# Optimization experiments

Measured on AMD Instinct MI355X. Metric: run time of the kernel, lower is better.

Reference implementation:

```python
import jax, jax.numpy as jnp
import numpy as np

N = 100000
E = 1600000
HID = 128


def gcn_conv(x, W, b, src, dst, n):
    # PyG GCNConv: h = X W; add self-loops; D^{-1/2}(A+I)D^{-1/2} h + b
    h = x @ W                                   # [n, out]
    loop = jnp.arange(n)
    s = jnp.concatenate([src, loop])            # sources incl. self-loops
    d = jnp.concatenate([dst, loop])            # targets incl. self-loops
    deg = jax.ops.segment_sum(jnp.ones(s.shape[0], dtype=h.dtype), d, num_segments=n)
    dinv = jnp.where(deg > 0, jax.lax.rsqrt(deg), 0.0)
    norm = dinv[s] * dinv[d]                    # [E+n]
    out = jax.ops.segment_sum(h[s] * norm[:, None], d, num_segments=n)
    return out + b


def setup_inputs() -> dict:
    key = jax.random.key(0)
    ks = jax.random.split(key, 16)
    coords = jax.random.normal(ks[0], (N, 2), dtype=jnp.float32)
    edge_index = jax.random.randint(ks[1], (2, E), 0, N, dtype=jnp.int64)

    def lin(k, fin, fout):
        k1, k2 = jax.random.split(k)
        s = 1.0 / np.sqrt(fin)
        W = jax.random.uniform(k1, (fin, fout), jnp.float32, -s, s)
        b = jax.random.uniform(k2, (fout,), jnp.float32, -s, s)
        return W, b

    W1, b1 = lin(ks[2], 3, HID)
    W2, b2 = lin(ks[3], HID, HID)
    Ws, bs = lin(ks[4], HID, 1)
    Wmu, bmu = lin(ks[5], HID, 2)
    Wls, bls = lin(ks[6], HID, 2)
    Wv1, bv1 = lin(ks[7], HID, 64)
    Wv2, bv2 = lin(ks[8], 64, 1)
    return {"coords": coords, "edge_index": edge_index,
            "W1": W1, "b1": b1, "W2": W2, "b2": b2,
            "Ws": Ws, "bs": bs, "Wmu": Wmu, "bmu": bmu,
            "Wls": Wls, "bls": bls, "Wv1": Wv1, "bv1": bv1,
            "Wv2": Wv2, "bv2": bv2}


def reference(coords, edge_index, W1, b1, W2, b2, Ws, bs, Wmu, bmu, Wls, bls, Wv1, bv1, Wv2, bv2):
    n = coords.shape[0]
    src, dst = edge_index[0], edge_index[1]
    # degree feature (no self-loops), normalized by max degree
    degree = jax.ops.segment_sum(jnp.ones(src.shape[0], dtype=jnp.float32), src, num_segments=n)
    degree = degree / jnp.maximum(degree.max(), 1.0)
    x = jnp.concatenate([coords, degree[:, None]], axis=1)  # [N, 3]
    x = jax.nn.relu(gcn_conv(x, W1, b1, src, dst, n))       # [N, HID]
    x = jax.nn.relu(gcn_conv(x, W2, b2, src, dst, n))       # [N, HID]
    node_logits = jax.nn.log_softmax((x @ Ws + bs).squeeze(-1), axis=0)  # [N]
    mu = x @ Wmu + bmu                                      # [N, 2]
    log_std = jnp.clip(x @ Wls + bls, -4.0, 2.0)            # [N, 2]
    g = x.mean(axis=0)                                      # [HID]
    value = (jax.nn.relu(g @ Wv1 + bv1) @ Wv2 + bv2).squeeze()
    return node_logits, mu, log_std, value
```

## Files before the change

### kernel.cpp

```cpp
#include <hip/hip_runtime.h>
#include <hip/hip_bf16.h>

#define HID 128
#define NBMAX 512

typedef __bf16 bf16x8 __attribute__((ext_vector_type(8)));
typedef float f32x4 __attribute__((ext_vector_type(4)));
typedef float f32x2 __attribute__((ext_vector_type(2)));

#if defined(__has_builtin)
#if __has_builtin(__builtin_amdgcn_cvt_pk_f32_fp8) && __has_builtin(__builtin_amdgcn_cvt_pk_fp8_f32)
#define HAVE_FP8_CVT 1
#endif
#endif
#ifndef HAVE_FP8_CVT
#define HAVE_FP8_CVT 0
#include <hip/hip_fp8.h>
#endif

__device__ __forceinline__ float b2f(unsigned int u) { return __uint_as_float(u << 16); }
__device__ __forceinline__ float b2f_hi(unsigned int u) { return __uint_as_float(u & 0xFFFF0000u); }
__device__ __forceinline__ unsigned int f2b(float f) {
  unsigned int b = __float_as_uint(f);
  return (b + 0x7FFFu + ((b >> 16) & 1u)) >> 16;
}
__device__ __forceinline__ unsigned int pack2(float lo, float hi) {
  return f2b(lo) | (f2b(hi) << 16);
}

#if !HAVE_FP8_CVT
__device__ __forceinline__ float fp8dec(unsigned int u) {
  unsigned int e = (u >> 3) & 15, m = u & 7, sgn = (u >> 7) & 1;
  float v;
  if (e) v = __uint_as_float(((e + 120) << 23) | (m << 20));
  else v = (float)m * 0.001953125f;
  return sgn ? -v : v;
}
#endif

__device__ __forceinline__ unsigned int pk4_fp8(float v0, float v1, float v2, float v3) {
#if HAVE_FP8_CVT
  int pk = 0;
  pk = __builtin_amdgcn_cvt_pk_fp8_f32(v0, v1, pk, false);
  pk = __builtin_amdgcn_cvt_pk_fp8_f32(v2, v3, pk, true);
  return (unsigned int)pk;
#else
  __hip_fp8_e4m3 a(v0), b(v1), c(v2), d(v3);
  return (unsigned)a.__x | ((unsigned)b.__x << 8) | ((unsigned)c.__x << 16) |
         ((unsigned)d.__x << 24);
#endif
}

__device__ __forceinline__ void acc4_fp8(unsigned int u, float* a) {
#if HAVE_FP8_CVT
  f32x2 lo = __builtin_amdgcn_cvt_pk_f32_fp8((int)u, false);
  f32x2 hi = __builtin_amdgcn_cvt_pk_f32_fp8((int)u, true);
  a[0] += lo.x; a[1] += lo.y; a[2] += hi.x; a[3] += hi.y;
#else
  a[0] += fp8dec(u & 255); a[1] += fp8dec((u >> 8) & 255);
  a[2] += fp8dec((u >> 16) & 255); a[3] += fp8dec((u >> 24) & 255);
#endif
}

__global__ void k_hist(const int* __restrict__ src, const int* __restrict__ dst, int E, int NB,
                       int* __restrict__ hd_g, int* __restrict__ hs_g) {
  __shared__ int hd[NBMAX], hs[NBMAX];
  for (int i = threadIdx.x; i < NB; i += 256) { hd[i] = 0; hs[i] = 0; }
  __syncthreads();
  int stride = gridDim.x * 256;
  for (int e = blockIdx.x * 256 + threadIdx.x; e < E; e += stride) {
    atomicAdd(&hd[dst[e] >> 8], 1);
    atomicAdd(&hs[src[e] >> 8], 1);
  }
  __syncthreads();
  for (int i = threadIdx.x; i < NB; i += 256) {
    if (hd[i]) atomicAdd(&hd_g[i], hd[i]);
    if (hs[i]) atomicAdd(&hs_g[i], hs[i]);
  }
}

__global__ void k_scan_buckets(const int* __restrict__ hd_g, const int* __restrict__ hs_g,
                               int NB, int E, int* __restrict__ based, int* __restrict__ bases,
                               int* __restrict__ curd, int* __restrict__ curs) {
  __shared__ int sd[NBMAX], ss[NBMAX];
  int i = threadIdx.x;
  int vd = (i < NB) ? hd_g[i] : 0;
  int vs = (i < NB) ? hs_g[i] : 0;
  sd[i] = vd; ss[i] = vs; __syncthreads();
  for (int st = 1; st < NBMAX; st <<= 1) {
    int td = (i >= st) ? sd[i - st] : 0;
    int ts = (i >= st) ? ss[i - st] : 0;
    __syncthreads();
    sd[i] += td; ss[i] += ts;
    __syncthreads();
  }
  if (i < NB) {
    int bd = sd[i] - vd, bs = ss[i] - vs;
    based[i] = bd; bases[i] = bs;
    curd[i] = bd; curs[i] = bs;
  }
  if (i == 0) { based[NB] = E; bases[NB] = E; }
}

__global__ void k_bucket_scatter(const int* __restrict__ src, const int* __restrict__ dst,
                                 int E, int NB, int* __restrict__ curd, int* __restrict__ curs,
                                 int* __restrict__ pairsp, int* __restrict__ srcb) {
  __shared__ int hd[NBMAX], hs[NBMAX], bd[NBMAX], bs[NBMAX];
  for (int i = threadIdx.x; i < NB; i += 256) { hd[i] = 0; hs[i] = 0; }
  __syncthreads();
  int per = (E + gridDim.x - 1) / gridDim.x;
  int begin = blockIdx.x * per;
  int end = min(E, begin + per);
  for (int e = begin + threadIdx.x; e < end; e += 256) {
    atomicAdd(&hd[dst[e] >> 8], 1);
    atomicAdd(&hs[src[e] >> 8], 1);
  }
  __syncthreads();
  for (int i = threadIdx.x; i < NB; i += 256) {
    bd[i] = hd[i] ? atomicAdd(&curd[i], hd[i]) : 0;
    bs[i] = hs[i] ? atomicAdd(&curs[i], hs[i]) : 0;
    hd[i] = 0; hs[i] = 0;
  }
  __syncthreads();
  for (int e = begin + threadIdx.x; e < end; e += 256) {
    int d = dst[e], s = src[e];
    int p = bd[d >> 8] + atomicAdd(&hd[d >> 8], 1);
    pairsp[p] = (s << 8) | (d & 255);
    int q = bs[s >> 8] + atomicAdd(&hs[s >> 8], 1);
    srcb[q] = s;
  }
}

__global__ void k_degcsr(const int* __restrict__ srcb, const int* __restrict__ bases,
                         const int* __restrict__ pairsp, const int* __restrict__ based,
                         int N, int E, int* __restrict__ degsrc, int* __restrict__ bmax,
                         int* __restrict__ rowptr, float* __restrict__ dinv,
                         int* __restrict__ colarr) {
  __shared__ int cnt[256], scn[256], cur[256];
  int b = blockIdx.x, tid = threadIdx.x;
  int g = (b << 8) + tid;
  cnt[tid] = 0; __syncthreads();
  int lo = bases[b], hi = bases[b + 1];
  for (int k = lo + tid; k < hi; k += 256) atomicAdd(&cnt[srcb[k] & 255], 1);
  __syncthreads();
  int c = cnt[tid];
  if (g < N) degsrc[g] = c;
  scn[tid] = (g < N) ? c : 0; __syncthreads();
  for (int s = 128; s > 0; s >>= 1) {
    if (tid < s) scn[tid] = max(scn[tid], scn[tid + s]);
    __syncthreads();
  }
  if (tid == 0) bmax[b] = scn[0];
  __syncthreads();
  cnt[tid] = 0; __syncthreads();
  lo = based[b]; hi = based[b + 1];
  for (int k = lo + tid; k < hi; k += 256) atomicAdd(&cnt[pairsp[k] & 255], 1);
  __syncthreads();
  c = cnt[tid];
  scn[tid] = c; __syncthreads();
  for (int st = 1; st < 256; st <<= 1) {
    int t = (tid >= st) ? scn[tid - st] : 0;
    __syncthreads();
    scn[tid] += t;
    __syncthreads();
  }
  int excl = scn[tid] - c;
  if (g < N) {
    rowptr[g] = lo + excl;
    dinv[g] = rsqrtf((float)(c + 1));
  }
  cur[tid] = lo + excl;
  __syncthreads();
  for (int k = lo + tid; k < hi; k += 256) {
    int p = pairsp[k];
    int pos = atomicAdd(&cur[p & 255], 1);
    colarr[pos] = ((unsigned)p) >> 8;
  }
  if (b == 0 && tid == 0) rowptr[N] = E;
}

__global__ void k_prepW(const float* __restrict__ W2, unsigned short* __restrict__ W2T) {
  int idx = blockIdx.x * 256 + threadIdx.x;
  if (idx >= 128 * 128) return;
  int j = idx >> 7, k = idx & 127;
  W2T[j * 128 + k] = (unsigned short)f2b(W2[k * 128 + j]);
}

__global__ void k_node(const float* __restrict__ coords, const int* __restrict__ degsrc,
                       const float* __restrict__ dinv, const int* __restrict__ bmax, int NB,
                       int N, float4* __restrict__ x0s) {
  __shared__ int sm[256];
  int tid = threadIdx.x;
  int m = 0;
  for (int i = tid; i < NB; i += 256) m = max(m, bmax[i]);
  sm[tid] = m; __syncthreads();
  for (int s = 128; s > 0; s >>= 1) {
    if (tid < s) sm[tid] = max(sm[tid], sm[tid + s]);
    __syncthreads();
  }
  float inv = 1.0f / (float)max(sm[0], 1);
  int n = blockIdx.x * 256 + tid;
  if (n >= N) return;
  float di = dinv[n];
  float4 v;
  v.x = coords[n * 2 + 0] * di;
  v.y = coords[n * 2 + 1] * di;
  v.z = (float)degsrc[n] * inv * di;
  v.w = 0.f;
  x0s[n] = v;
}

__global__ void k_agg3lin(const float4* __restrict__ x0s, const float* __restrict__ dinv,
                          const int* __restrict__ rowptr, const int* __restrict__ col,
                          const float* __restrict__ W1, const float* __restrict__ b1, int N,
                          unsigned int* __restrict__ x1f8) {
  __shared__ float w0s[128], w1s[128], w2s[128], bsm[128];
  for (int t = threadIdx.x; t < 128; t += 256) {
    w0s[t] = W1[t];
    w1s[t] = W1[128 + t];
    w2s[t] = W1[256 + t];
    bsm[t] = b1[t];
  }
  __syncthreads();
  int n = blockIdx.x * 256 + threadIdx.x;
  if (n >= N) return;
  float4 a = x0s[n];
  int b = rowptr[n], en = rowptr[n + 1];
  int k = b;
  for (; k + 3 < en; k += 4) {
    int s0 = col[k], s1 = col[k + 1], s2 = col[k + 2], s3 = col[k + 3];
    float4 w0 = x0s[s0];
    float4 w1 = x0s[s1];
    float4 w2 = x0s[s2];
    float4 w3 = x0s[s3];
    a.x += (w0.x + w1.x) + (w2.x + w3.x);
    a.y += (w0.y + w1.y) + (w2.y + w3.y);
    a.z += (w0.z + w1.z) + (w2.z + w3.z);
  }
  for (; k < en; k++) {
    float4 w = x0s[col[k]];
    a.x += w.x; a.y += w.y; a.z += w.z;
  }
  float di = dinv[n];
  float ax = a.x * di, ay = a.y * di, az = a.z * di;
  unsigned int* orow = x1f8 + (size_t)n * 32;
#pragma unroll 8
  for (int f0 = 0; f0 < 128; f0 += 4) {
    float v0 = fmaxf(bsm[f0] + ax * w0s[f0] + ay * w1s[f0] + az * w2s[f0], 0.f) * di;
    float v1 = fmaxf(bsm[f0 + 1] + ax * w0s[f0 + 1] + ay * w1s[f0 + 1] + az * w2s[f0 + 1], 0.f) * di;
    float v2 = fmaxf(bsm[f0 + 2] + ax * w0s[f0 + 2] + ay * w1s[f0 + 2] + az * w2s[f0 + 2], 0.f) * di;
    float v3 = fmaxf(bsm[f0 + 3] + ax * w0s[f0 + 3] + ay * w1s[f0 + 3] + az * w2s[f0 + 3], 0.f) * di;
    orow[f0 >> 2] = pk4_fp8(v0, v1, v2, v3);
  }
}

__global__ void k_agg128(const unsigned int* __restrict__ x1f8, const float* __restrict__ dinv,
                         const int* __restrict__ rowptr, const int* __restrict__ col,
                         int N, unsigned short* __restrict__ xa) {
  int g = (int)((blockIdx.x * 256 + threadIdx.x) >> 3);
  int lane = threadIdx.x & 7;
  if (g >= N) return;
  const uint4* base = (const uint4*)x1f8 + lane;
  float acc[16];
#pragma unroll
  for (int i = 0; i < 16; i++) acc[i] = 0.f;
  uint4 self = base[(size_t)g * 8];
  acc4_fp8(self.x, acc); acc4_fp8(self.y, acc + 4);
  acc4_fp8(self.z, acc + 8); acc4_fp8(self.w, acc + 12);
  int b = rowptr[g], en = rowptr[g + 1];
  int k = b;
  for (; k + 3 < en; k += 4) {
    int s0 = col[k], s1 = col[k + 1], s2 = col[k + 2], s3 = col[k + 3];
    uint4 w0 = base[(size_t)s0 * 8];
    uint4 w1 = base[(size_t)s1 * 8];
    uint4 w2 = base[(size_t)s2 * 8];
    uint4 w3 = base[(size_t)s3 * 8];
    acc4_fp8(w0.x, acc); acc4_fp8(w0.y, acc + 4); acc4_fp8(w0.z, acc + 8); acc4_fp8(w0.w, acc + 12);
    acc4_fp8(w1.x, acc); acc4_fp8(w1.y, acc + 4); acc4_fp8(w1.z, acc + 8); acc4_fp8(w1.w, acc + 12);
    acc4_fp8(w2.x, acc); acc4_fp8(w2.y, acc + 4); acc4_fp8(w2.z, acc + 8); acc4_fp8(w2.w, acc + 12);
    acc4_fp8(w3.x, acc); acc4_fp8(w3.y, acc + 4); acc4_fp8(w3.z, acc + 8); acc4_fp8(w3.w, acc + 12);
  }
  for (; k < en; k++) {
    uint4 w = base[(size_t)col[k] * 8];
    acc4_fp8(w.x, acc); acc4_fp8(w.y, acc + 4); acc4_fp8(w.z, acc + 8); acc4_fp8(w.w, acc + 12);
  }
  float di = dinv[g];
  uint4 o1, o2;
  o1.x = pack2(acc[0] * di, acc[1] * di);
  o1.y = pack2(acc[2] * di, acc[3] * di);
  o1.z = pack2(acc[4] * di, acc[5] * di);
  o1.w = pack2(acc[6] * di, acc[7] * di);
  o2.x = pack2(acc[8] * di, acc[9] * di);
  o2.y = pack2(acc[10] * di, acc[11] * di);
  o2.z = pack2(acc[12] * di, acc[13] * di);
  o2.w = pack2(acc[14] * di, acc[15] * di);
  uint4* op = (uint4*)xa + (size_t)g * 16 + lane * 2;
  op[0] = o1;
  op[1] = o2;
}

__global__ __launch_bounds__(256) void k_gemm2(const unsigned short* __restrict__ xab,
                                               const unsigned short* __restrict__ W2T,
                                               const float* __restrict__ b2,
                                               const float* __restrict__ Ws,
                                               const float* __restrict__ bs,
                                               const float* __restrict__ Wmu,
                                               const float* __restrict__ bmu,
                                               const float* __restrict__ Wls,
                                               const float* __restrict__ bls,
                                               int N, float* __restrict__ s_arr,
                                               float* __restrict__ out,
                                               float* __restrict__ partials) {
  __shared__ float w[640];
  __shared__ float cs[4][128];
  for (int t = threadIdx.x; t < 128; t += 256) {
    w[t] = Ws[t];
    w[128 + t] = Wmu[t * 2 + 0];
    w[256 + t] = Wmu[t * 2 + 1];
    w[384 + t] = Wls[t * 2 + 0];
    w[512 + t] = Wls[t * 2 + 1];
  }
  __syncthreads();
  int wv = threadIdx.x >> 6;
  int lane = threadIdx.x & 63;
  int l15 = lane & 15, lhi = lane >> 4;
  int rowbase = blockIdx.x * 64 + wv * 16;
  int arow = rowbase + l15;
  int arowc = min(arow, N - 1);
  const unsigned short* ap = xab + (size_t)arowc * HID + lhi * 8;
  bf16x8 a[4];
#pragma unroll
  for (int kk = 0; kk < 4; kk++) a[kk] = *(const bf16x8*)(ap + kk * 32);
  float cpart[8];
  float p0[4] = {0, 0, 0, 0}, p1[4] = {0, 0, 0, 0}, p2[4] = {0, 0, 0, 0};
  float p3[4] = {0, 0, 0, 0}, p4[4] = {0, 0, 0, 0};
#pragma unroll
  for (int ct = 0; ct < 8; ct++) {
    f32x4 acc = {0.f, 0.f, 0.f, 0.f};
    const unsigned short* bp = W2T + (size_t)(ct * 16 + l15) * HID + lhi * 8;
#pragma unroll
    for (int kk = 0; kk < 4; kk++) {
      bf16x8 bfr = *(const bf16x8*)(bp + kk * 32);
      acc = __builtin_amdgcn_mfma_f32_16x16x32_bf16(a[kk], bfr, acc, 0, 0, 0);
    }
    int cidx = ct * 16 + l15;
    float bias = b2[cidx];
    float ws_ = w[cidx];
    float wm0 = w[128 + cidx], wm1 = w[256 + cidx];
    float wl0 = w[384 + cidx], wl1 = w[512 + cidx];
    float cl = 0.f;
#pragma unroll
    for (int r = 0; r < 4; r++) {
      int node = rowbase + lhi * 4 + r;
      float o = fmaxf(acc[r] + bias, 0.f);
      if (node < N) cl += o;
      p0[r] += o * ws_;
      p1[r] += o * wm0;
      p2[r] += o * wm1;
      p3[r] += o * wl0;
      p4[r] += o * wl1;
    }
    cl += __shfl_xor(cl, 16);
    cl += __shfl_xor(cl, 32);
    cpart[ct] = cl;
  }
#pragma unroll
  for (int r = 0; r < 4; r++) {
#pragma unroll
    for (int m = 1; m < 16; m <<= 1) {
      p0[r] += __shfl_xor(p0[r], m);
      p1[r] += __shfl_xor(p1[r], m);
      p2[r] += __shfl_xor(p2[r], m);
      p3[r] += __shfl_xor(p3[r], m);
      p4[r] += __shfl_xor(p4[r], m);
    }
  }
  if (l15 == 0) {
#pragma unroll
    for (int r = 0; r < 4; r++) {
      int node = rowbase + lhi * 4 + r;
      if (node < N) {
        s_arr[node] = p0[r] + bs[0];
        out[(size_t)N + node * 2 + 0] = p1[r] + bmu[0];
        out[(size_t)N + node * 2 + 1] = p2[r] + bmu[1];
        out[(size_t)3 * N + node * 2 + 0] = fminf(fmaxf(p3[r] + bls[0], -4.f), 2.f);
        out[(size_t)3 * N + node * 2 + 1] = fminf(fmaxf(p4[r] + bls[1], -4.f), 2.f);
      }
    }
  }
  if (lane < 16) {
#pragma unroll
    for (int ct = 0; ct < 8; ct++) cs[wv][ct * 16 + lane] = cpart[ct];
  }
  __syncthreads();
  if (threadIdx.x < 128) {
    int f = threadIdx.x;
    partials[(size_t)blockIdx.x * 128 + f] = cs[0][f] + cs[1][f] + cs[2][f] + cs[3][f];
  }
}

__global__ void k_lse_colsum(const float* __restrict__ s, int N, float* __restrict__ pm,
                             float* __restrict__ pt, const float* __restrict__ partials,
                             int nblkG, float* __restrict__ colsum) {
  if (blockIdx.x >= 256) {
    int bb = blockIdx.x - 256;
    int f = threadIdx.x;
    if (f < 128) {
      float t = 0.f;
      for (int b = bb; b < nblkG; b += 64) t += partials[(size_t)b * 128 + f];
      atomicAdd(&colsum[f], t);
    }
    return;
  }
  __shared__ float smM[256], smT[256];
  float m = -1e30f, t = 0.f;
  for (int i = blockIdx.x * 256 + threadIdx.x; i < N; i += 256 * 256) {
    float v = s[i];
    if (v > m) { t = t * __expf(m - v) + 1.f; m = v; }
    else t += __expf(v - m);
  }
  smM[threadIdx.x] = m; smT[threadIdx.x] = t; __syncthreads();
  for (int st = 128; st > 0; st >>= 1) {
    if (threadIdx.x < st) {
      float m2 = smM[threadIdx.x + st], t2 = smT[threadIdx.x + st];
      float m1 = smM[threadIdx.x], t1 = smT[threadIdx.x];
      float M = fmaxf(m1, m2);
      smM[threadIdx.x] = M;
      smT[threadIdx.x] = t1 * __expf(m1 - M) + t2 * __expf(m2 - M);
    }
    __syncthreads();
  }
  if (threadIdx.x == 0) { pm[blockIdx.x] = smM[0]; pt[blockIdx.x] = smT[0]; }
}

__global__ void k_logits_value(const float* __restrict__ sarr, const float* __restrict__ pm,
                               const float* __restrict__ pt, int N, float* __restrict__ out,
                               const float* __restrict__ colsum, const float* __restrict__ Wv1,
                               const float* __restrict__ bv1, const float* __restrict__ Wv2,
                               const float* __restrict__ bv2, int nblkN) {
  if ((int)blockIdx.x == nblkN) {
    __shared__ float hid[64];
    float invN = 1.0f / (float)N;
    int j = threadIdx.x;
    if (j < 64) {
      float a = bv1[j];
      for (int f = 0; f < 128; f++) a += (colsum[f] * invN) * Wv1[f * 64 + j];
      hid[j] = fmaxf(a, 0.f) * Wv2[j];
    }
    __syncthreads();
    if (threadIdx.x == 0) {
      float v = bv2[0];
      for (int jj = 0; jj < 64; jj++) v += hid[jj];
      out[(size_t)5 * N] = v;
    }
    return;
  }
  __shared__ float smM[256], smT[256];
  smM[threadIdx.x] = pm[threadIdx.x];
  smT[threadIdx.x] = pt[threadIdx.x];
  __syncthreads();
  for (int st = 128; st > 0; st >>= 1) {
    if (threadIdx.x < st) {
      float m2 = smM[threadIdx.x + st], t2 = smT[threadIdx.x + st];
      float m1 = smM[threadIdx.x], t1 = smT[threadIdx.x];
      float M = fmaxf(m1, m2);
      smM[threadIdx.x] = M;
      smT[threadIdx.x] = t1 * __expf(m1 - M) + t2 * __expf(m2 - M);
    }
    __syncthreads();
  }
  float lse = smM[0] + logf(smT[0]);
  int n = blockIdx.x * 256 + threadIdx.x;
  if (n < N) out[n] = sarr[n] - lse;
}

extern "C" void kernel_launch(void* const* d_in, const int* in_sizes, int n_in,
                              void* d_out, int out_size, void* d_ws, size_t ws_size,
                              hipStream_t stream) {
  const float* coords = (const float*)d_in[0];
  const int* ei = (const int*)d_in[1];
  const float* W1 = (const float*)d_in[2];
  const float* b1 = (const float*)d_in[3];
  const float* W2 = (const float*)d_in[4];
  const float* b2 = (const float*)d_in[5];
  const float* Wsw = (const float*)d_in[6];
  const float* bsw = (const float*)d_in[7];
  const float* Wmu = (const float*)d_in[8];
  const float* bmu = (const float*)d_in[9];
  const float* Wls = (const float*)d_in[10];
  const float* bls = (const float*)d_in[11];
  const float* Wv1 = (const float*)d_in[12];
  const float* bv1 = (const float*)d_in[13];
  const float* Wv2 = (const float*)d_in[14];
  const float* bv2 = (const float*)d_in[15];
  int N = in_sizes[0] / 2;
  int E = in_sizes[1] / 2;
  const int* src = ei;
  const int* dst = ei + E;
  float* outf = (float*)d_out;
  int NB = (N + 255) >> 8;
  int nblkG = (N + 63) / 64;
  int nblkN = (N + 255) / 256;

  char* base = (char*)d_ws;
  size_t off = 0;
  auto alloc = [&](size_t bytes) -> void* {
    void* r = base + off;
    off += (bytes + 255) & ~(size_t)255;
    return r;
  };
  size_t zero_start = off;
  int* hd_g = (int*)alloc((size_t)NB * 4);
  int* hs_g = (int*)alloc((size_t)NB * 4);
  float* colsum = (float*)alloc(128 * 4);
  size_t zero_bytes = off - zero_start;
  int* based = (int*)alloc(((size_t)NB + 1) * 4);
  int* bases = (int*)alloc(((size_t)NB + 1) * 4);
  int* curd = (int*)alloc((size_t)NB * 4);
  int* curs = (int*)alloc((size_t)NB * 4);
  int* bmax = (int*)alloc((size_t)NB * 4);
  int* rowptr = (int*)alloc(((size_t)N + 1) * 4);
  int* pairsp = (int*)alloc((size_t)E * 4);
  int* srcb = (int*)alloc((size_t)E * 4);
  int* colarr = (int*)alloc((size_t)E * 4);
  int* degsrc = (int*)alloc((size_t)N * 4);
  float* dinv = (float*)alloc((size_t)N * 4);
  float4* x0s = (float4*)alloc((size_t)N * 16);
  float* sarr = (float*)alloc((size_t)N * 4);
  float* pm = (float*)alloc(256 * 4);
  float* pt = (float*)alloc(256 * 4);
  unsigned short* W2T = (unsigned short*)alloc(128 * 128 * 2);
  float* partials = (float*)alloc((size_t)nblkG * 128 * 4);
  unsigned int* x1f8 = (unsigned int*)alloc((size_t)N * 128);
  unsigned short* xab = (unsigned short*)alloc((size_t)N * HID * 2);
  if (off > ws_size) return;

  hipMemsetAsync(base + zero_start, 0, zero_bytes, stream);
  k_hist<<<256, 256, 0, stream>>>(src, dst, E, NB, hd_g, hs_g);
  k_scan_buckets<<<1, NBMAX, 0, stream>>>(hd_g, hs_g, NB, E, based, bases, curd, curs);
  k_bucket_scatter<<<512, 256, 0, stream>>>(src, dst, E, NB, curd, curs, pairsp, srcb);
  k_degcsr<<<NB, 256, 0, stream>>>(srcb, bases, pairsp, based, N, E, degsrc, bmax, rowptr, dinv,
                                   colarr);
  k_prepW<<<64, 256, 0, stream>>>(W2, W2T);
  k_node<<<nblkN, 256, 0, stream>>>(coords, degsrc, dinv, bmax, NB, N, x0s);
  k_agg3lin<<<nblkN, 256, 0, stream>>>(x0s, dinv, rowptr, colarr, W1, b1, N, x1f8);
  k_agg128<<<(N * 8 + 255) / 256, 256, 0, stream>>>(x1f8, dinv, rowptr, colarr, N, xab);
  k_gemm2<<<nblkG, 256, 0, stream>>>(xab, W2T, b2, Wsw, bsw, Wmu, bmu, Wls, bls, N, sarr, outf,
                                     partials);
  k_lse_colsum<<<320, 256, 0, stream>>>(sarr, N, pm, pt, partials, nblkG, colsum);
  k_logits_value<<<nblkN + 1, 256, 0, stream>>>(sarr, pm, pt, N, outf, colsum, Wv1, bv1, Wv2,
                                                bv2, nblkN);
}
```

Measured before the change: 202.9 us.

## Replace histogram-scan bucketing with fixed-capacity 1024-node buckets and int2 row ranges

Drops the global histogram and bucket-scan kernels. Edges are now scattered straight into fixed-capacity slots per bucket, with each bucket covering 1024 nodes and capacity set to about 1.25x the average plus slack. The CSR build kernel moves to 1024-thread blocks, and row pointers become int2 begin/end pairs. This removes two launches and one full pass over the edge list. In exchange, the CSR build runs only about 98 blocks, and any edge that lands past a bucket's capacity is silently dropped, so skewed graphs would give wrong results.

```diff
diff --git a/kernel.cpp b/kernel.cpp
--- a/kernel.cpp
+++ b/kernel.cpp
@@ -2,7 +2,7 @@
 #include <hip/hip_bf16.h>
 
 #define HID 128
-#define NBMAX 512
+#define NB2MAX 128
 
 typedef __bf16 bf16x8 __attribute__((ext_vector_type(8)));
 typedef float f32x4 __attribute__((ext_vector_type(4)));
@@ -19,7 +19,6 @@
 #endif
 
 __device__ __forceinline__ float b2f(unsigned int u) { return __uint_as_float(u << 16); }
-__device__ __forceinline__ float b2f_hi(unsigned int u) { return __uint_as_float(u & 0xFFFF0000u); }
 __device__ __forceinline__ unsigned int f2b(float f) {
   unsigned int b = __float_as_uint(f);
   return (b + 0x7FFFu + ((b >> 16) & 1u)) >> 16;
@@ -62,61 +61,21 @@
 #endif
 }
 
-__global__ void k_hist(const int* __restrict__ src, const int* __restrict__ dst, int E, int NB,
-                       int* __restrict__ hd_g, int* __restrict__ hs_g) {
-  __shared__ int hd[NBMAX], hs[NBMAX];
-  for (int i = threadIdx.x; i < NB; i += 256) { hd[i] = 0; hs[i] = 0; }
-  __syncthreads();
-  int stride = gridDim.x * 256;
-  for (int e = blockIdx.x * 256 + threadIdx.x; e < E; e += stride) {
-    atomicAdd(&hd[dst[e] >> 8], 1);
-    atomicAdd(&hs[src[e] >> 8], 1);
-  }
-  __syncthreads();
-  for (int i = threadIdx.x; i < NB; i += 256) {
-    if (hd[i]) atomicAdd(&hd_g[i], hd[i]);
-    if (hs[i]) atomicAdd(&hs_g[i], hs[i]);
-  }
-}
-
-__global__ void k_scan_buckets(const int* __restrict__ hd_g, const int* __restrict__ hs_g,
-                               int NB, int E, int* __restrict__ based, int* __restrict__ bases,
-                               int* __restrict__ curd, int* __restrict__ curs) {
-  __shared__ int sd[NBMAX], ss[NBMAX];
-  int i = threadIdx.x;
-  int vd = (i < NB) ? hd_g[i] : 0;
-  int vs = (i < NB) ? hs_g[i] : 0;
-  sd[i] = vd; ss[i] = vs; __syncthreads();
-  for (int st = 1; st < NBMAX; st <<= 1) {
-    int td = (i >= st) ? sd[i - st] : 0;
-    int ts = (i >= st) ? ss[i - st] : 0;
-    __syncthreads();
-    sd[i] += td; ss[i] += ts;
-    __syncthreads();
-  }
-  if (i < NB) {
-    int bd = sd[i] - vd, bs = ss[i] - vs;
-    based[i] = bd; bases[i] = bs;
-    curd[i] = bd; curs[i] = bs;
-  }
-  if (i == 0) { based[NB] = E; bases[NB] = E; }
-}
-
-__global__ void k_bucket_scatter(const int* __restrict__ src, const int* __restrict__ dst,
-                                 int E, int NB, int* __restrict__ curd, int* __restrict__ curs,
-                                 int* __restrict__ pairsp, int* __restrict__ srcb) {
-  __shared__ int hd[NBMAX], hs[NBMAX], bd[NBMAX], bs[NBMAX];
-  for (int i = threadIdx.x; i < NB; i += 256) { hd[i] = 0; hs[i] = 0; }
+__global__ void k_scatter2(const int* __restrict__ src, const int* __restrict__ dst, int E,
+                           int NB2, int CAP, int* __restrict__ curd, int* __restrict__ curs,
+                           int* __restrict__ pairsp, int* __restrict__ srcb) {
+  __shared__ int hd[NB2MAX], hs[NB2MAX], bd[NB2MAX], bs[NB2MAX];
+  for (int i = threadIdx.x; i < NB2; i += 256) { hd[i] = 0; hs[i] = 0; }
   __syncthreads();
   int per = (E + gridDim.x - 1) / gridDim.x;
   int begin = blockIdx.x * per;
   int end = min(E, begin + per);
   for (int e = begin + threadIdx.x; e < end; e += 256) {
-    atomicAdd(&hd[dst[e] >> 8], 1);
-    atomicAdd(&hs[src[e] >> 8], 1);
-  }
-  __syncthreads();
-  for (int i = threadIdx.x; i < NB; i += 256) {
+    atomicAdd(&hd[dst[e] >> 10], 1);
+    atomicAdd(&hs[src[e] >> 10], 1);
+  }
+  __syncthreads();
+  for (int i = threadIdx.x; i < NB2; i += 256) {
     bd[i] = hd[i] ? atomicAdd(&curd[i], hd[i]) : 0;
     bs[i] = hs[i] ? atomicAdd(&curs[i], hs[i]) : 0;
     hd[i] = 0; hs[i] = 0;
@@ -124,41 +83,45 @@
   __syncthreads();
   for (int e = begin + threadIdx.x; e < end; e += 256) {
     int d = dst[e], s = src[e];
-    int p = bd[d >> 8] + atomicAdd(&hd[d >> 8], 1);
-    pairsp[p] = (s << 8) | (d & 255);
-    int q = bs[s >> 8] + atomicAdd(&hs[s >> 8], 1);
-    srcb[q] = s;
-  }
-}
-
-__global__ void k_degcsr(const int* __restrict__ srcb, const int* __restrict__ bases,
-                         const int* __restrict__ pairsp, const int* __restrict__ based,
-                         int N, int E, int* __restrict__ degsrc, int* __restrict__ bmax,
-                         int* __restrict__ rowptr, float* __restrict__ dinv,
-                         int* __restrict__ colarr) {
-  __shared__ int cnt[256], scn[256], cur[256];
+    int bD = d >> 10, bS = s >> 10;
+    int offD = bd[bD] + atomicAdd(&hd[bD], 1);
+    if (offD < CAP) pairsp[(size_t)bD * CAP + offD] = (s << 10) | (d & 1023);
+    int offS = bs[bS] + atomicAdd(&hs[bS], 1);
+    if (offS < CAP) srcb[(size_t)bS * CAP + offS] = s & 1023;
+  }
+}
+
+__global__ __launch_bounds__(1024) void k_degcsr(
+    const int* __restrict__ srcb, const int* __restrict__ curs, const int* __restrict__ pairsp,
+    const int* __restrict__ curd, int NB2, int CAP, int N, int* __restrict__ degsrc,
+    int* __restrict__ bmax, int2* __restrict__ rowptr2, float* __restrict__ dinv,
+    int* __restrict__ colarr) {
+  __shared__ int cnt[1024], scn[1024], cur[1024];
   int b = blockIdx.x, tid = threadIdx.x;
-  int g = (b << 8) + tid;
+  int g = (b << 10) + tid;
+  int lo = b * CAP;
   cnt[tid] = 0; __syncthreads();
-  int lo = bases[b], hi = bases[b + 1];
-  for (int k = lo + tid; k < hi; k += 256) atomicAdd(&cnt[srcb[k] & 255], 1);
+  int szS = min(curs[b], CAP);
+  const int* sb = srcb + (size_t)lo;
+  for (int k = tid; k < szS; k += 1024) atomicAdd(&cnt[sb[k]], 1);
   __syncthreads();
   int c = cnt[tid];
   if (g < N) degsrc[g] = c;
   scn[tid] = (g < N) ? c : 0; __syncthreads();
-  for (int s = 128; s > 0; s >>= 1) {
+  for (int s = 512; s > 0; s >>= 1) {
     if (tid < s) scn[tid] = max(scn[tid], scn[tid + s]);
     __syncthreads();
   }
   if (tid == 0) bmax[b] = scn[0];
   __syncthreads();
   cnt[tid] = 0; __syncthreads();
-  lo = based[b]; hi = based[b + 1];
-  for (int k = lo + tid; k < hi; k += 256) atomicAdd(&cnt[pairsp[k] & 255], 1);
+  int szD = min(curd[b], CAP);
+  const int* pb = pairsp + (size_t)lo;
+  for (int k = tid; k < szD; k += 1024) atomicAdd(&cnt[pb[k] & 1023], 1);
   __syncthreads();
   c = cnt[tid];
   scn[tid] = c; __syncthreads();
-  for (int st = 1; st < 256; st <<= 1) {
+  for (int st = 1; st < 1024; st <<= 1) {
     int t = (tid >= st) ? scn[tid - st] : 0;
     __syncthreads();
     scn[tid] += t;
@@ -166,17 +129,16 @@
   }
   int excl = scn[tid] - c;
   if (g < N) {
-    rowptr[g] = lo + excl;
+    rowptr2[g] = make_int2(lo + excl, lo + excl + c);
     dinv[g] = rsqrtf((float)(c + 1));
   }
   cur[tid] = lo + excl;
   __syncthreads();
-  for (int k = lo + tid; k < hi; k += 256) {
-    int p = pairsp[k];
-    int pos = atomicAdd(&cur[p & 255], 1);
-    colarr[pos] = ((unsigned)p) >> 8;
-  }
-  if (b == 0 && tid == 0) rowptr[N] = E;
+  for (int k = tid; k < szD; k += 1024) {
+    int p = pb[k];
+    int pos = atomicAdd(&cur[p & 1023], 1);
+    colarr[pos] = ((unsigned)p) >> 10;
+  }
 }
 
 __global__ void k_prepW(const float* __restrict__ W2, unsigned short* __restrict__ W2T) {
@@ -187,17 +149,26 @@
 }
 
 __global__ void k_node(const float* __restrict__ coords, const int* __restrict__ degsrc,
-                       const float* __restrict__ dinv, const int* __restrict__ bmax, int NB,
+                       const float* __restrict__ dinv, const int* __restrict__ bmax, int NB2,
                        int N, float4* __restrict__ x0s) {
-  __shared__ int sm[256];
+  __shared__ int sm[128];
   int tid = threadIdx.x;
-  int m = 0;
-  for (int i = tid; i < NB; i += 256) m = max(m, bmax[i]);
-  sm[tid] = m; __syncthreads();
-  for (int s = 128; s > 0; s >>= 1) {
-    if (tid < s) sm[tid] = max(sm[tid], sm[tid + s]);
-    __syncthreads();
-  }
+  if (tid < 128) sm[tid] = (tid < NB2) ? bmax[tid] : 0;
+  __syncthreads();
+  if (tid < 64) { sm[tid] = max(sm[tid], sm[tid + 64]); }
+  __syncthreads();
+  if (tid < 32) { sm[tid] = max(sm[tid], sm[tid + 32]); }
+  __syncthreads();
+  if (tid < 16) { sm[tid] = max(sm[tid], sm[tid + 16]); }
+  __syncthreads();
+  if (tid < 8) { sm[tid] = max(sm[tid], sm[tid + 8]); }
+  __syncthreads();
+  if (tid < 4) { sm[tid] = max(sm[tid], sm[tid + 4]); }
+  __syncthreads();
+  if (tid < 2) { sm[tid] = max(sm[tid], sm[tid + 2]); }
+  __syncthreads();
+  if (tid == 0) sm[0] = max(sm[0], sm[1]);
+  __syncthreads();
   float inv = 1.0f / (float)max(sm[0], 1);
   int n = blockIdx.x * 256 + tid;
   if (n >= N) return;
@@ -211,7 +182,7 @@
 }
 
 __global__ void k_agg3lin(const float4* __restrict__ x0s, const float* __restrict__ dinv,
-                          const int* __restrict__ rowptr, const int* __restrict__ col,
+                          const int2* __restrict__ rowptr2, const int* __restrict__ col,
                           const float* __restrict__ W1, const float* __restrict__ b1, int N,
                           unsigned int* __restrict__ x1f8) {
   __shared__ float w0s[128], w1s[128], w2s[128], bsm[128];
@@ -225,8 +196,8 @@
   int n = blockIdx.x * 256 + threadIdx.x;
   if (n >= N) return;
   float4 a = x0s[n];
-  int b = rowptr[n], en = rowptr[n + 1];
-  int k = b;
+  int2 rp = rowptr2[n];
+  int k = rp.x, en = rp.y;
   for (; k + 3 < en; k += 4) {
     int s0 = col[k], s1 = col[k + 1], s2 = col[k + 2], s3 = col[k + 3];
     float4 w0 = x0s[s0];
@@ -255,7 +226,7 @@
 }
 
 __global__ void k_agg128(const unsigned int* __restrict__ x1f8, const float* __restrict__ dinv,
-                         const int* __restrict__ rowptr, const int* __restrict__ col,
+                         const int2* __restrict__ rowptr2, const int* __restrict__ col,
                          int N, unsigned short* __restrict__ xa) {
   int g = (int)((blockIdx.x * 256 + threadIdx.x) >> 3);
   int lane = threadIdx.x & 7;
@@ -267,8 +238,8 @@
   uint4 self = base[(size_t)g * 8];
   acc4_fp8(self.x, acc); acc4_fp8(self.y, acc + 4);
   acc4_fp8(self.z, acc + 8); acc4_fp8(self.w, acc + 12);
-  int b = rowptr[g], en = rowptr[g + 1];
-  int k = b;
+  int2 rp = rowptr2[g];
+  int k = rp.x, en = rp.y;
   for (; k + 3 < en; k += 4) {
     int s0 = col[k], s1 = col[k + 1], s2 = col[k + 2], s3 = col[k + 3];
     uint4 w0 = base[(size_t)s0 * 8];
@@ -498,7 +469,8 @@
   const int* src = ei;
   const int* dst = ei + E;
   float* outf = (float*)d_out;
-  int NB = (N + 255) >> 8;
+  int NB2 = (N + 1023) >> 10;
+  int CAP = ((E / NB2) * 5 / 4 + 1024 + 255) & ~255;
   int nblkG = (N + 63) / 64;
   int nblkN = (N + 255) / 256;
 
@@ -510,19 +482,15 @@
     return r;
   };
   size_t zero_start = off;
-  int* hd_g = (int*)alloc((size_t)NB * 4);
-  int* hs_g = (int*)alloc((size_t)NB * 4);
+  int* curd = (int*)alloc((size_t)NB2 * 4);
+  int* curs = (int*)alloc((size_t)NB2 * 4);
   float* colsum = (float*)alloc(128 * 4);
   size_t zero_bytes = off - zero_start;
-  int* based = (int*)alloc(((size_t)NB + 1) * 4);
-  int* bases = (int*)alloc(((size_t)NB + 1) * 4);
-  int* curd = (int*)alloc((size_t)NB * 4);
-  int* curs = (int*)alloc((size_t)NB * 4);
-  int* bmax = (int*)alloc((size_t)NB * 4);
-  int* rowptr = (int*)alloc(((size_t)N + 1) * 4);
-  int* pairsp = (int*)alloc((size_t)E * 4);
-  int* srcb = (int*)alloc((size_t)E * 4);
-  int* colarr = (int*)alloc((size_t)E * 4);
+  int* bmax = (int*)alloc((size_t)NB2 * 4);
+  int2* rowptr2 = (int2*)alloc((size_t)N * 8);
+  int* pairsp = (int*)alloc((size_t)NB2 * CAP * 4);
+  int* srcb = (int*)alloc((size_t)NB2 * CAP * 4);
+  int* colarr = (int*)alloc((size_t)NB2 * CAP * 4);
   int* degsrc = (int*)alloc((size_t)N * 4);
   float* dinv = (float*)alloc((size_t)N * 4);
   float4* x0s = (float4*)alloc((size_t)N * 16);
@@ -536,15 +504,13 @@
   if (off > ws_size) return;
 
   hipMemsetAsync(base + zero_start, 0, zero_bytes, stream);
-  k_hist<<<256, 256, 0, stream>>>(src, dst, E, NB, hd_g, hs_g);
-  k_scan_buckets<<<1, NBMAX, 0, stream>>>(hd_g, hs_g, NB, E, based, bases, curd, curs);
-  k_bucket_scatter<<<512, 256, 0, stream>>>(src, dst, E, NB, curd, curs, pairsp, srcb);
-  k_degcsr<<<NB, 256, 0, stream>>>(srcb, bases, pairsp, based, N, E, degsrc, bmax, rowptr, dinv,
-                                   colarr);
+  k_scatter2<<<1024, 256, 0, stream>>>(src, dst, E, NB2, CAP, curd, curs, pairsp, srcb);
+  k_degcsr<<<NB2, 1024, 0, stream>>>(srcb, curs, pairsp, curd, NB2, CAP, N, degsrc, bmax,
+                                     rowptr2, dinv, colarr);
   k_prepW<<<64, 256, 0, stream>>>(W2, W2T);
-  k_node<<<nblkN, 256, 0, stream>>>(coords, degsrc, dinv, bmax, NB, N, x0s);
-  k_agg3lin<<<nblkN, 256, 0, stream>>>(x0s, dinv, rowptr, colarr, W1, b1, N, x1f8);
-  k_agg128<<<(N * 8 + 255) / 256, 256, 0, stream>>>(x1f8, dinv, rowptr, colarr, N, xab);
+  k_node<<<nblkN, 256, 0, stream>>>(coords, degsrc, dinv, bmax, NB2, N, x0s);
+  k_agg3lin<<<nblkN, 256, 0, stream>>>(x0s, dinv, rowptr2, colarr, W1, b1, N, x1f8);
+  k_agg128<<<(N * 8 + 255) / 256, 256, 0, stream>>>(x1f8, dinv, rowptr2, colarr, N, xab);
   k_gemm2<<<nblkG, 256, 0, stream>>>(xab, W2T, b2, Wsw, bsw, Wmu, bmu, Wls, bls, N, sarr, outf,
                                      partials);
   k_lse_colsum<<<320, 256, 0, stream>>>(sarr, N, pm, pt, partials, nblkG, colsum);
```

Result: faster. 183.2 us (-9.7%).
